# Optimization experiments

Hardware: AMD Instinct MI355X
Metric: run time of the kernel (lower is better)

The kernel has to match this reference:

```python
import jax, jax.numpy as jnp
import numpy as np
import math

# Static module config (matches init_kwargs)
C = 1.0            # ball curvature parameter c
IN_C, OUT_C = 512, 512
K, PAD = 3, 1
T, B = 2048, 16
EPS = 1e-15
RC = math.sqrt(C)

def _beta(a, b):
    return math.exp(math.lgamma(a) + math.lgamma(b) - math.lgamma(a + b))

BETA_NI = _beta(IN_C / 2.0, 0.5)            # beta(n_i/2, 1/2)
BETA_N = _beta(IN_C * K / 2.0, 0.5)         # beta(n/2, 1/2)
BETA_RATIO = BETA_N / BETA_NI
PROJ_EPS = 4e-3                              # geoopt float32 projection eps


def logmap0(y):
    # y in Poincare ball -> tangent at origin
    yn = jnp.clip(jnp.linalg.norm(y, axis=-1, keepdims=True), EPS, None)
    arg = jnp.clip(RC * yn, None, 1.0 - 1e-7)
    return y * (jnp.arctanh(arg) / (RC * yn))


def expmap0(u):
    un = jnp.clip(jnp.linalg.norm(u, axis=-1, keepdims=True), EPS, None)
    return jnp.tanh(RC * un) * u / (RC * un)


def project(x):
    maxnorm = (1.0 - PROJ_EPS) / RC
    norm = jnp.clip(jnp.linalg.norm(x, axis=-1, keepdims=True), EPS, None)
    return x * jnp.where(norm > maxnorm, maxnorm / norm, 1.0)


def poincare_linear(x, w_g, w_unit, b):
    # unidirectional Poincare MLR (geoopt_plusplus)
    rcx = RC * x                                             # [T,B,K*Cin]
    cx2 = jnp.sum(rcx * rcx, axis=-1, keepdims=True)         # [T,B,1]
    drcr = 2.0 * RC * b                                      # [Cout]
    num = 2.0 * jnp.einsum('tbi,io->tbo', rcx, w_unit) * jnp.cosh(drcr) \
          - (1.0 + cx2) * jnp.sinh(drcr)
    y = (2.0 * w_g / RC) * jnp.arcsinh(num / jnp.clip(1.0 - cx2, EPS, None))
    y = jnp.sinh(RC * y) / RC
    denom = 1.0 + jnp.sqrt(1.0 + C * jnp.sum(y * y, axis=-1, keepdims=True))
    return project(y / denom)


def setup_inputs() -> dict:
    key = jax.random.key(0)
    k1, k2, k3 = jax.random.split(key, 3)
    # points strictly inside the unit ball: ||x|| < 0.7
    v = jax.random.normal(k1, (T, B, IN_C), dtype=jnp.float32)
    vn = jnp.linalg.norm(v, axis=-1, keepdims=True)
    x = v / (1.0 + vn) * 0.7
    std = (2.0 * IN_C * K * OUT_C) ** -0.5
    w = jax.random.normal(k2, (K * IN_C, OUT_C), dtype=jnp.float32) * std
    weight_g = jnp.clip(jnp.linalg.norm(w, axis=0), 1e-15, None)   # [Cout]
    weight_v = w / weight_g                                        # [K*Cin, Cout]
    bias = jnp.zeros((OUT_C,), dtype=jnp.float32)
    return {"x": x, "weight_g": weight_g, "weight_v": weight_v, "bias": bias}


def reference(x, weight_g, weight_v, bias):
    u = logmap0(x) * BETA_RATIO                 # tangent space, rescaled
    u = jnp.pad(u, ((PAD, PAD), (0, 0), (0, 0)))
    olen = u.shape[0] - K + 1
    # im2col over time: [olen, B, K*Cin]
    u = jnp.concatenate([u[k:k + olen] for k in range(K)], axis=-1)
    xh = expmap0(u)
    w_unit = weight_v / jnp.clip(jnp.linalg.norm(weight_v, axis=0), EPS, None)
    return poincare_linear(xh, weight_g, w_unit, bias)
```

## Files before the change

### kernel.cpp

```cpp
#include <hip/hip_runtime.h>
#include <cstdint>
#include <cmath>

typedef unsigned short u16;
typedef short bf16x8 __attribute__((ext_vector_type(8)));
typedef float f32x4 __attribute__((ext_vector_type(4)));

#define T_DIM 2048
#define B_DIM 16
#define CIN 512
#define COUT 512
#define KIN 1536
#define NROWS (T_DIM * B_DIM)
#define UROWS ((T_DIM + 2) * B_DIM)

#define NS 48

#define LOG2E 1.44269504088896f
#define LN2   0.69314718055995f

__device__ __forceinline__ float fast_exp2(float x) {
#if __has_builtin(__builtin_amdgcn_exp2f)
  return __builtin_amdgcn_exp2f(x);
#else
  return __builtin_exp2f(x);
#endif
}
__device__ __forceinline__ float fast_log2(float x) {
#if __has_builtin(__builtin_amdgcn_logf)
  return __builtin_amdgcn_logf(x);
#else
  return __builtin_log2f(x);
#endif
}
__device__ __forceinline__ float fast_rcp(float x) {
  return __builtin_amdgcn_rcpf(x);
}

__device__ __forceinline__ u16 f2bf(float f) {
  unsigned u = __builtin_bit_cast(unsigned, f);
  u = (u + 0x7FFFu + ((u >> 16) & 1u)) >> 16;
  return (u16)u;
}

typedef __attribute__((address_space(3))) unsigned int as3u32;
typedef __attribute__((address_space(1))) unsigned int as1u32;

__device__ __forceinline__ void gload16(const u16* g, const u16* lds) {
#if __has_builtin(__builtin_amdgcn_global_load_lds)
  __builtin_amdgcn_global_load_lds((as1u32*)(uintptr_t)g,
                                   (as3u32*)(unsigned)(uintptr_t)lds, 16, 0, 0);
#else
  unsigned lane = __lane_id();
  ((uint4*)lds)[lane] = *(const uint4*)g;
#endif
}

__global__ __launch_bounds__(256) void k_colnorm(const float* __restrict__ wv,
                                                 float* __restrict__ partial) {
  int o = blockIdx.x * 256 + threadIdx.x;
  int r0 = blockIdx.y * 64;
  float s = 0.f;
#pragma unroll 8
  for (int r = 0; r < 64; ++r) {
    float v = wv[(size_t)(r0 + r) * COUT + o];
    s += v * v;
  }
  partial[(size_t)blockIdx.y * COUT + o] = s;
}

__global__ __launch_bounds__(256) void k_fin(const float* __restrict__ partial,
                                             const float* __restrict__ bias,
                                             float* __restrict__ invn,
                                             float* __restrict__ ch,
                                             float* __restrict__ sh) {
  int o = blockIdx.x * 256 + threadIdx.x;
  float s = 0.f;
#pragma unroll
  for (int j = 0; j < KIN / 64; ++j) s += partial[(size_t)j * COUT + o];
  invn[o] = 1.f / fmaxf(sqrtf(s), 1e-15f);
  float d = 2.f * bias[o];
  float e = fast_exp2(d * LOG2E);
  float ie = fast_rcp(e);
  ch[o] = 0.5f * (e + ie);
  sh[o] = 0.5f * (e - ie);
}

__global__ void k_wt(const float* __restrict__ wv, const float* __restrict__ invn,
                     u16* __restrict__ wt) {
  __shared__ float tile[64][65];
  int i0 = blockIdx.x * 64;
  int o0 = blockIdx.y * 64;
  int tx = threadIdx.x & 63, ty = threadIdx.x >> 6;
  for (int r = ty; r < 64; r += 4)
    tile[r][tx] = wv[(size_t)(i0 + r) * COUT + o0 + tx];
  __syncthreads();
  for (int r = ty; r < 64; r += 4) {
    float inv = invn[o0 + r];
    wt[(size_t)(o0 + r) * KIN + i0 + tx] = f2bf(tile[tx][r] * inv);
  }
}

__global__ void k_logmap(const float* __restrict__ x, u16* __restrict__ U,
                         float* __restrict__ nsq, float beta_ratio) {
  int row = blockIdx.x;
  int t = row >> 4;
  int lane = threadIdx.x;
  uint4* urow = (uint4*)(U + (size_t)row * CIN);
  if (t == 0 || t == T_DIM + 1) {
    uint4 z; z.x = z.y = z.z = z.w = 0u;
    urow[lane] = z;
    if (lane == 0) nsq[row] = 0.f;
    return;
  }
  const float4* xr = (const float4*)(x + (size_t)(row - 16) * CIN);
  float4 a = xr[lane * 2];
  float4 b = xr[lane * 2 + 1];
  float s = a.x*a.x + a.y*a.y + a.z*a.z + a.w*a.w
          + b.x*b.x + b.y*b.y + b.z*b.z + b.w*b.w;
#pragma unroll
  for (int d = 1; d < 64; d <<= 1) s += __shfl_xor(s, d);
  float r = sqrtf(s);
  float yn = fmaxf(r, 1e-15f);
  float arg = fminf(yn, 1.0f - 1e-7f);
  float at = 0.5f * LN2 * fast_log2((1.f + arg) * fast_rcp(1.f - arg));
  float f = at / yn * beta_ratio;
  union { u16 h[8]; uint4 v; } pk;
  pk.h[0] = f2bf(a.x * f); pk.h[1] = f2bf(a.y * f);
  pk.h[2] = f2bf(a.z * f); pk.h[3] = f2bf(a.w * f);
  pk.h[4] = f2bf(b.x * f); pk.h[5] = f2bf(b.y * f);
  pk.h[6] = f2bf(b.z * f); pk.h[7] = f2bf(b.w * f);
  urow[lane] = pk.v;
  if (lane == 0) nsq[row] = s * f * f;
}

__global__ __launch_bounds__(512, 2) void k_gemm(const u16* __restrict__ U,
                                                 const u16* __restrict__ WT,
                                                 const float* __restrict__ nsq,
                                                 const float* __restrict__ wg,
                                                 const float* __restrict__ chv,
                                                 const float* __restrict__ shv,
                                                 float* __restrict__ out) {
  __shared__ u16 lA[3][128 * 32];
  __shared__ u16 lB[3][512 * 32];
  int bm = blockIdx.x;
  int tid = threadIdx.x;
  int lane = tid & 63;
  int wid = tid >> 6;
  int wr = wid >> 2, wc = wid & 3;
  int lr = lane & 15;
  int sc = (tid & 3) ^ ((tid >> 3) & 3);
  int cSwz = ((lane >> 4) ^ ((lr >> 1) & 3)) << 3;
  int ldsOffA = (wr * 64 + lr) * 32 + cSwz;
  int ldsOffB = (wc * 128 + lr) * 32 + cSwz;

  f32x4 acc[4][8] = {};

  auto stgA = [&](const u16* g, int p) {
    gload16(g, &lA[p][wid * 512]);
  };
  auto stgB = [&](const u16* g, int p) {
#pragma unroll
    for (int r = 0; r < 4; ++r)
      gload16(g + (size_t)r * (128 * KIN), &lB[p][r * 4096 + wid * 512]);
  };

  const u16* gA = U + (size_t)(bm * 128 + (tid >> 2)) * 512 + sc * 8;
  const u16* gB = WT + (size_t)(tid >> 2) * KIN + sc * 8;

  stgA(gA, 0);      stgB(gB, 0);
  stgA(gA + 32, 1); stgB(gB + 32, 1);
  gA += 64; gB += 64;
  asm volatile("s_waitcnt vmcnt(5)" ::: "memory");
  asm volatile("s_barrier" ::: "memory");

  for (int tt = 0; tt < 16; ++tt) {
#pragma unroll
    for (int u = 0; u < 3; ++u) {
      int t = tt * 3 + u;
      int b = u;
      int p = (u + 2) % 3;
      if (t + 2 < NS) {
        stgA(gA, p); stgB(gB, p);
        int t2 = t + 2;
        gA += ((t2 & 15) == 15) ? 7712 : 32;
        gB += 32;
      }
      const u16* pA = &lA[b][ldsOffA];
      const u16* pB = &lB[b][ldsOffB];
      bf16x8 af[4], bf[8];
#pragma unroll
      for (int i = 0; i < 4; ++i) af[i] = *(const bf16x8*)(pA + i * 512);
#pragma unroll
      for (int i = 0; i < 8; ++i) bf[i] = *(const bf16x8*)(pB + i * 512);
      __builtin_amdgcn_s_setprio(1);
#pragma unroll
      for (int mi = 0; mi < 4; ++mi)
#pragma unroll
        for (int ni = 0; ni < 8; ++ni)
          acc[mi][ni] = __builtin_amdgcn_mfma_f32_16x16x32_bf16(
              af[mi], bf[ni], acc[mi][ni], 0, 0, 0);
      __builtin_amdgcn_s_setprio(0);
      asm volatile("s_waitcnt lgkmcnt(0)" ::: "memory");
      if (t < NS - 2)       asm volatile("s_waitcnt vmcnt(5)" ::: "memory");
      else if (t == NS - 2) asm volatile("s_waitcnt vmcnt(0)" ::: "memory");
      asm volatile("s_barrier" ::: "memory");
    }
  }

  float* scr = (float*)&lA[0][0];
  float* scl = scr + 128 * 4;

  float g8[8], c8[8], s8[8];
#pragma unroll
  for (int ni = 0; ni < 8; ++ni) {
    int col = wc * 128 + ni * 16 + lr;
    g8[ni] = wg[col]; c8[ni] = chv[col]; s8[ni] = shv[col];
  }
  int rbase_loc = wr * 64 + ((lane >> 4) << 2);
  int rbase_glb = bm * 128 + rbase_loc;

#pragma unroll
  for (int mi = 0; mi < 4; ++mi) {
    float r1a[4], r2a[4], ssq[4];
#pragma unroll
    for (int j = 0; j < 4; ++j) {
      int m = rbase_glb + mi * 16 + j;
      float un2 = nsq[m] + nsq[m + 16] + nsq[m + 32];
      float un = sqrtf(un2);
      float unc = fmaxf(un, 1e-15f);
      float e2 = fast_exp2(unc * (2.f * LOG2E));
      float th = (e2 - 1.f) * fast_rcp(e2 + 1.f);
      float sxp = th * fast_rcp(unc);
      float cx2 = sxp * sxp * un2;
      float iden = fast_rcp(fmaxf(1.f - cx2, 1e-15f));
      r1a[j] = 2.f * sxp * iden;
      r2a[j] = (1.f + cx2) * iden;
      ssq[j] = 0.f;
    }
#pragma unroll
    for (int ni = 0; ni < 8; ++ni) {
#pragma unroll
      for (int j = 0; j < 4; ++j) {
        float z = r1a[j] * acc[mi][ni][j] * c8[ni] - r2a[j] * s8[ni];
        float w = z + sqrtf(fmaf(z, z, 1.f));
        float l = fast_log2(w);
        float E = fast_exp2((2.f * g8[ni]) * l);
        float y = 0.5f * (E - fast_rcp(E));
        acc[mi][ni][j] = y;
        ssq[j] += y * y;
      }
    }
#pragma unroll
    for (int j = 0; j < 4; ++j) {
#pragma unroll
      for (int d = 1; d < 16; d <<= 1) ssq[j] += __shfl_xor(ssq[j], d);
    }
    if (lr == 0) {
#pragma unroll
      for (int j = 0; j < 4; ++j)
        scr[(rbase_loc + mi * 16 + j) * 4 + wc] = ssq[j];
    }
  }
  __syncthreads();
  if (tid < 128) {
    float ss = scr[tid * 4] + scr[tid * 4 + 1] + scr[tid * 4 + 2] + scr[tid * 4 + 3];
    float denom = 1.f + sqrtf(1.f + ss);
    float idn = 1.f / denom;
    float nrm = fmaxf(sqrtf(ss) * idn, 1e-15f);
    float maxn = 1.0f - 4e-3f;
    float scale = (nrm > maxn) ? (maxn / nrm) : 1.f;
    scl[tid] = scale * idn;
  }
  __syncthreads();

#pragma unroll
  for (int mi = 0; mi < 4; ++mi) {
    float sc4[4];
#pragma unroll
    for (int j = 0; j < 4; ++j) sc4[j] = scl[rbase_loc + mi * 16 + j];
#pragma unroll
    for (int ni = 0; ni < 8; ++ni) {
      int col = wc * 128 + ni * 16 + lr;
#pragma unroll
      for (int j = 0; j < 4; ++j)
        out[(size_t)(rbase_glb + mi * 16 + j) * COUT + col] = acc[mi][ni][j] * sc4[j];
    }
  }
}

extern "C" void kernel_launch(void* const* d_in, const int* in_sizes, int n_in,
                              void* d_out, int out_size, void* d_ws, size_t ws_size,
                              hipStream_t stream) {
  const float* x    = (const float*)d_in[0];
  const float* wg   = (const float*)d_in[1];
  const float* wv   = (const float*)d_in[2];
  const float* bias = (const float*)d_in[3];
  float* out = (float*)d_out;

  char* ws = (char*)d_ws;
  u16*   U    = (u16*)(ws);
  float* NSQ  = (float*)(ws + 33587200);
  u16*   WT   = (u16*)(ws + 33718400);
  float* INVN = (float*)(ws + 35291264);
  float* CH   = (float*)(ws + 35293312);
  float* SH   = (float*)(ws + 35295360);
  float* PART = (float*)(ws + 35297408);

  double lb = (lgamma(768.0) + lgamma(0.5) - lgamma(768.5))
            - (lgamma(256.0) + lgamma(0.5) - lgamma(256.5));
  float beta_ratio = (float)exp(lb);

  k_colnorm<<<dim3(COUT / 256, KIN / 64), 256, 0, stream>>>(wv, PART);
  k_fin<<<COUT / 256, 256, 0, stream>>>(PART, bias, INVN, CH, SH);
  k_wt<<<dim3(KIN / 64, COUT / 64), 256, 0, stream>>>(wv, INVN, WT);
  k_logmap<<<UROWS, 64, 0, stream>>>(x, U, NSQ, beta_ratio);
  k_gemm<<<NROWS / 128, 512, 0, stream>>>(U, WT, NSQ, wg, CH, SH, out);
}
```

Measured before the change: 104.4 us.

## Halve GEMM row tile, double-buffer LDS, and fold finalize kernel into neighbors

The GEMM block tile shrinks from 128 to 64 rows. All 8 waves now split the 512 output columns, and the A tile is staged with 4-byte LDS loads. The pipeline moves from triple to double buffering so LDS and registers fit four blocks per CU, which doubles the grid for better occupancy and load balance. The separate finalize kernel is removed: its cosh/sinh work goes into the column-norm kernel and the inverse-norm reduction into the transpose kernel, saving one launch. The cost is rereading WT twice as often per output and a shallower prefetch depth.

After: 118.5 us. +13.5%, slower.

```diff
diff --git a/kernel.cpp b/kernel.cpp
--- a/kernel.cpp
+++ b/kernel.cpp
@@ -55,9 +55,21 @@
   ((uint4*)lds)[lane] = *(const uint4*)g;
 #endif
 }
+__device__ __forceinline__ void gload4(const u16* g, const u16* lds) {
+#if __has_builtin(__builtin_amdgcn_global_load_lds)
+  __builtin_amdgcn_global_load_lds((as1u32*)(uintptr_t)g,
+                                   (as3u32*)(unsigned)(uintptr_t)lds, 4, 0, 0);
+#else
+  unsigned lane = __lane_id();
+  ((unsigned*)lds)[lane] = *(const unsigned*)g;
+#endif
+}
 
 __global__ __launch_bounds__(256) void k_colnorm(const float* __restrict__ wv,
-                                                 float* __restrict__ partial) {
+                                                 const float* __restrict__ bias,
+                                                 float* __restrict__ partial,
+                                                 float* __restrict__ ch,
+                                                 float* __restrict__ sh) {
   int o = blockIdx.x * 256 + threadIdx.x;
   int r0 = blockIdx.y * 64;
   float s = 0.f;
@@ -67,36 +79,33 @@
     s += v * v;
   }
   partial[(size_t)blockIdx.y * COUT + o] = s;
-}
-
-__global__ __launch_bounds__(256) void k_fin(const float* __restrict__ partial,
-                                             const float* __restrict__ bias,
-                                             float* __restrict__ invn,
-                                             float* __restrict__ ch,
-                                             float* __restrict__ sh) {
-  int o = blockIdx.x * 256 + threadIdx.x;
-  float s = 0.f;
-#pragma unroll
-  for (int j = 0; j < KIN / 64; ++j) s += partial[(size_t)j * COUT + o];
-  invn[o] = 1.f / fmaxf(sqrtf(s), 1e-15f);
-  float d = 2.f * bias[o];
-  float e = fast_exp2(d * LOG2E);
-  float ie = fast_rcp(e);
-  ch[o] = 0.5f * (e + ie);
-  sh[o] = 0.5f * (e - ie);
-}
-
-__global__ void k_wt(const float* __restrict__ wv, const float* __restrict__ invn,
+  if (blockIdx.y == 0) {
+    float d = 2.f * bias[o];
+    float e = fast_exp2(d * LOG2E);
+    float ie = fast_rcp(e);
+    ch[o] = 0.5f * (e + ie);
+    sh[o] = 0.5f * (e - ie);
+  }
+}
+
+__global__ void k_wt(const float* __restrict__ wv, const float* __restrict__ partial,
                      u16* __restrict__ wt) {
   __shared__ float tile[64][65];
+  __shared__ float invl[64];
   int i0 = blockIdx.x * 64;
   int o0 = blockIdx.y * 64;
   int tx = threadIdx.x & 63, ty = threadIdx.x >> 6;
+  if (threadIdx.x < 64) {
+    float s = 0.f;
+#pragma unroll
+    for (int j = 0; j < KIN / 64; ++j) s += partial[(size_t)j * COUT + o0 + threadIdx.x];
+    invl[threadIdx.x] = 1.f / fmaxf(sqrtf(s), 1e-15f);
+  }
   for (int r = ty; r < 64; r += 4)
     tile[r][tx] = wv[(size_t)(i0 + r) * COUT + o0 + tx];
   __syncthreads();
   for (int r = ty; r < 64; r += 4) {
-    float inv = invn[o0 + r];
+    float inv = invl[r];
     wt[(size_t)(o0 + r) * KIN + i0 + tx] = f2bf(tile[tx][r] * inv);
   }
 }
@@ -134,30 +143,34 @@
   if (lane == 0) nsq[row] = s * f * f;
 }
 
-__global__ __launch_bounds__(512, 2) void k_gemm(const u16* __restrict__ U,
+__global__ __launch_bounds__(512, 4) void k_gemm(const u16* __restrict__ U,
                                                  const u16* __restrict__ WT,
                                                  const float* __restrict__ nsq,
                                                  const float* __restrict__ wg,
                                                  const float* __restrict__ chv,
                                                  const float* __restrict__ shv,
                                                  float* __restrict__ out) {
-  __shared__ u16 lA[3][128 * 32];
-  __shared__ u16 lB[3][512 * 32];
+  __shared__ u16 lA[2][64 * 32];
+  __shared__ u16 lB[2][512 * 32];
   int bm = blockIdx.x;
   int tid = threadIdx.x;
   int lane = tid & 63;
   int wid = tid >> 6;
-  int wr = wid >> 2, wc = wid & 3;
   int lr = lane & 15;
-  int sc = (tid & 3) ^ ((tid >> 3) & 3);
+  int scB = (tid & 3) ^ ((tid >> 3) & 3);
+  int scA = ((tid >> 2) & 3) ^ ((tid >> 5) & 3);
   int cSwz = ((lane >> 4) ^ ((lr >> 1) & 3)) << 3;
-  int ldsOffA = (wr * 64 + lr) * 32 + cSwz;
-  int ldsOffB = (wc * 128 + lr) * 32 + cSwz;
-
-  f32x4 acc[4][8] = {};
+  int ldsOffA = lr * 32 + cSwz;
+  int ldsOffB = (wid * 64 + lr) * 32 + cSwz;
+
+  f32x4 acc[4][4] = {};
+
+  const u16* gA = U + (size_t)(bm * 64 + (tid >> 4)) * 512 + scA * 8 + (tid & 3) * 2;
+  const u16* gB = WT + (size_t)(tid >> 2) * KIN + scB * 8;
 
   auto stgA = [&](const u16* g, int p) {
-    gload16(g, &lA[p][wid * 512]);
+    gload4(g, &lA[p][wid * 128]);
+    gload4(g + 32 * 512, &lA[p][1024 + wid * 128]);
   };
   auto stgB = [&](const u16* g, int p) {
 #pragma unroll
@@ -165,60 +178,51 @@
       gload16(g + (size_t)r * (128 * KIN), &lB[p][r * 4096 + wid * 512]);
   };
 
-  const u16* gA = U + (size_t)(bm * 128 + (tid >> 2)) * 512 + sc * 8;
-  const u16* gB = WT + (size_t)(tid >> 2) * KIN + sc * 8;
-
-  stgA(gA, 0);      stgB(gB, 0);
-  stgA(gA + 32, 1); stgB(gB + 32, 1);
-  gA += 64; gB += 64;
-  asm volatile("s_waitcnt vmcnt(5)" ::: "memory");
-  asm volatile("s_barrier" ::: "memory");
-
-  for (int tt = 0; tt < 16; ++tt) {
-#pragma unroll
-    for (int u = 0; u < 3; ++u) {
-      int t = tt * 3 + u;
-      int b = u;
-      int p = (u + 2) % 3;
-      if (t + 2 < NS) {
-        stgA(gA, p); stgB(gB, p);
-        int t2 = t + 2;
-        gA += ((t2 & 15) == 15) ? 7712 : 32;
-        gB += 32;
-      }
-      const u16* pA = &lA[b][ldsOffA];
-      const u16* pB = &lB[b][ldsOffB];
-      bf16x8 af[4], bf[8];
-#pragma unroll
-      for (int i = 0; i < 4; ++i) af[i] = *(const bf16x8*)(pA + i * 512);
-#pragma unroll
-      for (int i = 0; i < 8; ++i) bf[i] = *(const bf16x8*)(pB + i * 512);
-      __builtin_amdgcn_s_setprio(1);
-#pragma unroll
-      for (int mi = 0; mi < 4; ++mi)
-#pragma unroll
-        for (int ni = 0; ni < 8; ++ni)
-          acc[mi][ni] = __builtin_amdgcn_mfma_f32_16x16x32_bf16(
-              af[mi], bf[ni], acc[mi][ni], 0, 0, 0);
-      __builtin_amdgcn_s_setprio(0);
-      asm volatile("s_waitcnt lgkmcnt(0)" ::: "memory");
-      if (t < NS - 2)       asm volatile("s_waitcnt vmcnt(5)" ::: "memory");
-      else if (t == NS - 2) asm volatile("s_waitcnt vmcnt(0)" ::: "memory");
-      asm volatile("s_barrier" ::: "memory");
-    }
+  stgA(gA, 0); stgB(gB, 0);
+  gA += 32; gB += 32;
+
+  for (int t = 0; t < NS; ++t) {
+    int b = t & 1;
+    if (t + 1 < NS) {
+      stgA(gA, b ^ 1); stgB(gB, b ^ 1);
+      int s = t + 1;
+      gA += ((s & 15) == 15) ? 7712 : 32;
+      gB += 32;
+      asm volatile("s_waitcnt vmcnt(6)" ::: "memory");
+    } else {
+      asm volatile("s_waitcnt vmcnt(0)" ::: "memory");
+    }
+    asm volatile("s_barrier" ::: "memory");
+    const u16* pA = &lA[b][ldsOffA];
+    const u16* pB = &lB[b][ldsOffB];
+    bf16x8 af[4], bf[4];
+#pragma unroll
+    for (int i = 0; i < 4; ++i) af[i] = *(const bf16x8*)(pA + i * 512);
+#pragma unroll
+    for (int i = 0; i < 4; ++i) bf[i] = *(const bf16x8*)(pB + i * 512);
+    __builtin_amdgcn_s_setprio(1);
+#pragma unroll
+    for (int mi = 0; mi < 4; ++mi)
+#pragma unroll
+      for (int ni = 0; ni < 4; ++ni)
+        acc[mi][ni] = __builtin_amdgcn_mfma_f32_16x16x32_bf16(
+            af[mi], bf[ni], acc[mi][ni], 0, 0, 0);
+    __builtin_amdgcn_s_setprio(0);
+    asm volatile("s_waitcnt lgkmcnt(0)" ::: "memory");
+    asm volatile("s_barrier" ::: "memory");
   }
 
   float* scr = (float*)&lA[0][0];
-  float* scl = scr + 128 * 4;
-
-  float g8[8], c8[8], s8[8];
-#pragma unroll
-  for (int ni = 0; ni < 8; ++ni) {
-    int col = wc * 128 + ni * 16 + lr;
-    g8[ni] = wg[col]; c8[ni] = chv[col]; s8[ni] = shv[col];
-  }
-  int rbase_loc = wr * 64 + ((lane >> 4) << 2);
-  int rbase_glb = bm * 128 + rbase_loc;
+  float* scl = scr + 64 * 8;
+
+  float g4[4], c4[4], s4[4];
+#pragma unroll
+  for (int ni = 0; ni < 4; ++ni) {
+    int col = wid * 64 + ni * 16 + lr;
+    g4[ni] = wg[col]; c4[ni] = chv[col]; s4[ni] = shv[col];
+  }
+  int rbase_loc = (lane >> 4) << 2;
+  int rbase_glb = bm * 64 + rbase_loc;
 
 #pragma unroll
   for (int mi = 0; mi < 4; ++mi) {
@@ -239,13 +243,13 @@
       ssq[j] = 0.f;
     }
 #pragma unroll
-    for (int ni = 0; ni < 8; ++ni) {
+    for (int ni = 0; ni < 4; ++ni) {
 #pragma unroll
       for (int j = 0; j < 4; ++j) {
-        float z = r1a[j] * acc[mi][ni][j] * c8[ni] - r2a[j] * s8[ni];
+        float z = r1a[j] * acc[mi][ni][j] * c4[ni] - r2a[j] * s4[ni];
         float w = z + sqrtf(fmaf(z, z, 1.f));
         float l = fast_log2(w);
-        float E = fast_exp2((2.f * g8[ni]) * l);
+        float E = fast_exp2((2.f * g4[ni]) * l);
         float y = 0.5f * (E - fast_rcp(E));
         acc[mi][ni][j] = y;
         ssq[j] += y * y;
@@ -259,12 +263,14 @@
     if (lr == 0) {
 #pragma unroll
       for (int j = 0; j < 4; ++j)
-        scr[(rbase_loc + mi * 16 + j) * 4 + wc] = ssq[j];
+        scr[(rbase_loc + mi * 16 + j) * 8 + wid] = ssq[j];
     }
   }
   __syncthreads();
-  if (tid < 128) {
-    float ss = scr[tid * 4] + scr[tid * 4 + 1] + scr[tid * 4 + 2] + scr[tid * 4 + 3];
+  if (tid < 64) {
+    float ss = 0.f;
+#pragma unroll
+    for (int w = 0; w < 8; ++w) ss += scr[tid * 8 + w];
     float denom = 1.f + sqrtf(1.f + ss);
     float idn = 1.f / denom;
     float nrm = fmaxf(sqrtf(ss) * idn, 1e-15f);
@@ -280,8 +286,8 @@
 #pragma unroll
     for (int j = 0; j < 4; ++j) sc4[j] = scl[rbase_loc + mi * 16 + j];
 #pragma unroll
-    for (int ni = 0; ni < 8; ++ni) {
-      int col = wc * 128 + ni * 16 + lr;
+    for (int ni = 0; ni < 4; ++ni) {
+      int col = wid * 64 + ni * 16 + lr;
 #pragma unroll
       for (int j = 0; j < 4; ++j)
         out[(size_t)(rbase_glb + mi * 16 + j) * COUT + col] = acc[mi][ni][j] * sc4[j];
@@ -302,18 +308,16 @@
   u16*   U    = (u16*)(ws);
   float* NSQ  = (float*)(ws + 33587200);
   u16*   WT   = (u16*)(ws + 33718400);
-  float* INVN = (float*)(ws + 35291264);
-  float* CH   = (float*)(ws + 35293312);
-  float* SH   = (float*)(ws + 35295360);
-  float* PART = (float*)(ws + 35297408);
+  float* CH   = (float*)(ws + 35291264);
+  float* SH   = (float*)(ws + 35293312);
+  float* PART = (float*)(ws + 35295360);
 
   double lb = (lgamma(768.0) + lgamma(0.5) - lgamma(768.5))
             - (lgamma(256.0) + lgamma(0.5) - lgamma(256.5));
   float beta_ratio = (float)exp(lb);
 
-  k_colnorm<<<dim3(COUT / 256, KIN / 64), 256, 0, stream>>>(wv, PART);
-  k_fin<<<COUT / 256, 256, 0, stream>>>(PART, bias, INVN, CH, SH);
-  k_wt<<<dim3(KIN / 64, COUT / 64), 256, 0, stream>>>(wv, INVN, WT);
+  k_colnorm<<<dim3(COUT / 256, KIN / 64), 256, 0, stream>>>(wv, bias, PART, CH, SH);
+  k_wt<<<dim3(KIN / 64, COUT / 64), 256, 0, stream>>>(wv, PART, WT);
   k_logmap<<<UROWS, 64, 0, stream>>>(x, U, NSQ, beta_ratio);
-  k_gemm<<<NROWS / 128, 512, 0, stream>>>(U, WT, NSQ, wg, CH, SH, out);
-}
+  k_gemm<<<NROWS / 64, 512, 0, stream>>>(U, WT, NSQ, wg, CH, SH, out);
+}
```

## Merge weight-prep and logmap kernels into one launch, fold finalize into colnorm

Applied to the files above, without the earlier changes.

Cuts the launch count from five to three. The cosh/sinh bias terms are now computed inside the column-norm kernel. The per-column inverse norm is recomputed per transpose block, and the weight transpose and logmap run as disjoint block ranges of a single prep kernel. The logmap part now packs four 64-thread rows into each 256-thread block, so fewer, larger blocks are launched. The aim is to remove launch gaps and small serialized kernels, at the cost of some redundant reduction of the partial sums.

Result: faster. 96.69 us (median of 2 runs) (-7.4%).

```diff
diff --git a/kernel.cpp b/kernel.cpp
--- a/kernel.cpp
+++ b/kernel.cpp
@@ -15,6 +15,8 @@
 #define UROWS ((T_DIM + 2) * B_DIM)
 
 #define NS 48
+#define NWTBLK 192
+#define NLOGBLK 8200
 
 #define LOG2E 1.44269504088896f
 #define LN2   0.69314718055995f
@@ -57,7 +59,10 @@
 }
 
 __global__ __launch_bounds__(256) void k_colnorm(const float* __restrict__ wv,
-                                                 float* __restrict__ partial) {
+                                                 const float* __restrict__ bias,
+                                                 float* __restrict__ partial,
+                                                 float* __restrict__ ch,
+                                                 float* __restrict__ sh) {
   int o = blockIdx.x * 256 + threadIdx.x;
   int r0 = blockIdx.y * 64;
   float s = 0.f;
@@ -67,45 +72,48 @@
     s += v * v;
   }
   partial[(size_t)blockIdx.y * COUT + o] = s;
-}
-
-__global__ __launch_bounds__(256) void k_fin(const float* __restrict__ partial,
-                                             const float* __restrict__ bias,
-                                             float* __restrict__ invn,
-                                             float* __restrict__ ch,
-                                             float* __restrict__ sh) {
-  int o = blockIdx.x * 256 + threadIdx.x;
-  float s = 0.f;
-#pragma unroll
-  for (int j = 0; j < KIN / 64; ++j) s += partial[(size_t)j * COUT + o];
-  invn[o] = 1.f / fmaxf(sqrtf(s), 1e-15f);
-  float d = 2.f * bias[o];
-  float e = fast_exp2(d * LOG2E);
-  float ie = fast_rcp(e);
-  ch[o] = 0.5f * (e + ie);
-  sh[o] = 0.5f * (e - ie);
-}
-
-__global__ void k_wt(const float* __restrict__ wv, const float* __restrict__ invn,
-                     u16* __restrict__ wt) {
-  __shared__ float tile[64][65];
-  int i0 = blockIdx.x * 64;
-  int o0 = blockIdx.y * 64;
-  int tx = threadIdx.x & 63, ty = threadIdx.x >> 6;
-  for (int r = ty; r < 64; r += 4)
-    tile[r][tx] = wv[(size_t)(i0 + r) * COUT + o0 + tx];
-  __syncthreads();
-  for (int r = ty; r < 64; r += 4) {
-    float inv = invn[o0 + r];
-    wt[(size_t)(o0 + r) * KIN + i0 + tx] = f2bf(tile[tx][r] * inv);
-  }
-}
-
-__global__ void k_logmap(const float* __restrict__ x, u16* __restrict__ U,
-                         float* __restrict__ nsq, float beta_ratio) {
-  int row = blockIdx.x;
+  if (blockIdx.y == 0) {
+    float d = 2.f * bias[o];
+    float e = fast_exp2(d * LOG2E);
+    float ie = fast_rcp(e);
+    ch[o] = 0.5f * (e + ie);
+    sh[o] = 0.5f * (e - ie);
+  }
+}
+
+__global__ __launch_bounds__(256) void k_prep(const float* __restrict__ x,
+                                              u16* __restrict__ U,
+                                              float* __restrict__ nsq,
+                                              float beta_ratio,
+                                              const float* __restrict__ wv,
+                                              const float* __restrict__ partial,
+                                              u16* __restrict__ wt) {
+  int blk = blockIdx.x;
+  if (blk < NWTBLK) {
+    __shared__ float tile[64][65];
+    __shared__ float invl[64];
+    int i0 = (blk % 24) * 64;
+    int o0 = (blk / 24) * 64;
+    int tx = threadIdx.x & 63, ty = threadIdx.x >> 6;
+    if (threadIdx.x < 64) {
+      float s = 0.f;
+#pragma unroll
+      for (int j = 0; j < KIN / 64; ++j)
+        s += partial[(size_t)j * COUT + o0 + threadIdx.x];
+      invl[threadIdx.x] = 1.f / fmaxf(sqrtf(s), 1e-15f);
+    }
+    for (int r = ty; r < 64; r += 4)
+      tile[r][tx] = wv[(size_t)(i0 + r) * COUT + o0 + tx];
+    __syncthreads();
+    for (int r = ty; r < 64; r += 4) {
+      float inv = invl[r];
+      wt[(size_t)(o0 + r) * KIN + i0 + tx] = f2bf(tile[tx][r] * inv);
+    }
+    return;
+  }
+  int row = (blk - NWTBLK) * 4 + (threadIdx.x >> 6);
   int t = row >> 4;
-  int lane = threadIdx.x;
+  int lane = threadIdx.x & 63;
   uint4* urow = (uint4*)(U + (size_t)row * CIN);
   if (t == 0 || t == T_DIM + 1) {
     uint4 z; z.x = z.y = z.z = z.w = 0u;
@@ -302,18 +310,15 @@
   u16*   U    = (u16*)(ws);
   float* NSQ  = (float*)(ws + 33587200);
   u16*   WT   = (u16*)(ws + 33718400);
-  float* INVN = (float*)(ws + 35291264);
-  float* CH   = (float*)(ws + 35293312);
-  float* SH   = (float*)(ws + 35295360);
-  float* PART = (float*)(ws + 35297408);
+  float* CH   = (float*)(ws + 35291264);
+  float* SH   = (float*)(ws + 35293312);
+  float* PART = (float*)(ws + 35295360);
 
   double lb = (lgamma(768.0) + lgamma(0.5) - lgamma(768.5))
             - (lgamma(256.0) + lgamma(0.5) - lgamma(256.5));
   float beta_ratio = (float)exp(lb);
 
-  k_colnorm<<<dim3(COUT / 256, KIN / 64), 256, 0, stream>>>(wv, PART);
-  k_fin<<<COUT / 256, 256, 0, stream>>>(PART, bias, INVN, CH, SH);
-  k_wt<<<dim3(KIN / 64, COUT / 64), 256, 0, stream>>>(wv, INVN, WT);
-  k_logmap<<<UROWS, 64, 0, stream>>>(x, U, NSQ, beta_ratio);
+  k_colnorm<<<dim3(COUT / 256, KIN / 64), 256, 0, stream>>>(wv, bias, PART, CH, SH);
+  k_prep<<<NWTBLK + NLOGBLK, 256, 0, stream>>>(x, U, NSQ, beta_ratio, wv, PART, WT);
   k_gemm<<<NROWS / 128, 512, 0, stream>>>(U, WT, NSQ, wg, CH, SH, out);
 }
```
